# Kernel optimization log

Measured on AMD Instinct MI355X. Metric: run time of the kernel, lower is better.

## Reference

```python
import jax, jax.numpy as jnp
import numpy as np

N_NODES = 50000
N_EDGES = 1600000
N_GRAPHS = 512
VOCAB = 1000
EMB = 32
HID = 64
N_CLASS = 2


def setup_inputs() -> dict:
    key = jax.random.key(0)
    ks = jax.random.split(key, 12)
    x_ids = jax.random.randint(ks[0], (N_NODES,), 0, VOCAB)
    edge_index = jax.random.randint(ks[1], (2, N_EDGES), 0, N_NODES)
    batch = jnp.sort(jax.random.randint(ks[2], (N_NODES,), 0, N_GRAPHS))
    def s(k, shape, fan):
        return jax.random.normal(k, shape, jnp.float32) * (1.0 / np.sqrt(fan))
    return {
        "x_ids": x_ids,
        "edge_index": edge_index,
        "batch": batch,
        "embed": s(ks[3], (VOCAB, EMB), EMB),
        "w1_l": s(ks[4], (EMB, HID), EMB),
        "b1": jnp.zeros((HID,), jnp.float32),
        "w1_r": s(ks[5], (EMB, HID), EMB),
        "w2_l": s(ks[6], (HID, HID), HID),
        "b2": jnp.zeros((HID,), jnp.float32),
        "w2_r": s(ks[7], (HID, HID), HID),
        "w_out": s(ks[8], (HID, N_CLASS), HID),
        "b_out": jnp.zeros((N_CLASS,), jnp.float32),
    }


def _sage(x, src, dst, w_l, b, w_r):
    # PyG SAGEConv (aggr='mean'): out = lin_l(mean_{j in N(i)} x_j) + lin_r(x_i)
    msg_sum = jax.ops.segment_sum(x[src], dst, num_segments=N_NODES)  # [N, d]
    deg = jax.ops.segment_sum(jnp.ones((src.shape[0],), x.dtype), dst,
                              num_segments=N_NODES)
    mean = msg_sum / jnp.maximum(deg, 1.0)[:, None]
    return mean @ w_l + b + x @ w_r


def reference(x_ids, edge_index, batch, embed, w1_l, b1, w1_r,
              w2_l, b2, w2_r, w_out, b_out):
    src, dst = edge_index[0], edge_index[1]
    x = embed[x_ids]                                  # [N, emb]
    x = jax.nn.relu(_sage(x, src, dst, w1_l, b1, w1_r))  # [N, hid]
    x = jax.nn.relu(_sage(x, src, dst, w2_l, b2, w2_r))  # [N, hid]
    # global_mean_pool over batch segments
    gsum = jax.ops.segment_sum(x, batch, num_segments=N_GRAPHS)
    gcnt = jax.ops.segment_sum(jnp.ones((N_NODES,), x.dtype), batch,
                               num_segments=N_GRAPHS)
    pooled = gsum / jnp.maximum(gcnt, 1.0)[:, None]   # [G, hid]
    return pooled @ w_out + b_out                     # [G, n_class]
```

## Files before the change

### kernel.cpp

```cpp
#include <hip/hip_runtime.h>
#include <hip/hip_bf16.h>

#define N_NODES 50000
#define N_EDGES 1600000
#define N_GRAPHS 512
#define VOCAB 1000
#define EMB 32
#define HID 64
#define N_CLASS 2

#define MAXDEG 96

#define NVEC (N_EDGES / 4)
#define SORT_VPB 1024
#define SORT_BLOCKS ((NVEC + SORT_VPB - 1) / SORT_VPB)
#define BSHIFT 7
#define BUCKET_NODES 128
#define NBUCK ((N_NODES + BUCKET_NODES - 1) / BUCKET_NODES)

#define E1_BLOCKS ((VOCAB * HID + 255) / 256)

#define AGG_THREADS (N_NODES * 8)
#define AGG_BLOCKS ((AGG_THREADS + 255) / 256)

#define L2P_BLOCKS 768
#define L2P_WAVES (L2P_BLOCKS * 4)
#define L2P_CHUNK ((N_NODES + L2P_WAVES - 1) / L2P_WAVES)

typedef int iv4 __attribute__((ext_vector_type(4)));
typedef unsigned short us;
typedef us usv8 __attribute__((ext_vector_type(8)));
typedef float fv4 __attribute__((ext_vector_type(4)));
typedef unsigned long long u64;

__device__ __forceinline__ float bf2f(us u) {
    union { unsigned int i; float f; } c;
    c.i = ((unsigned int)u) << 16;
    return c.f;
}
__device__ __forceinline__ us f2bf(float f) {
    union { __hip_bfloat16 b; us u; } c;
    c.b = __float2bfloat16(f);
    return c.u;
}
__device__ __forceinline__ float rdlane(float v, int k) {
    return __int_as_float(__builtin_amdgcn_readlane(__float_as_int(v), k));
}

__global__ __launch_bounds__(256) void pre_hist_kernel(
        const int* __restrict__ dst, int* __restrict__ hist,
        const float* __restrict__ embed, const float* __restrict__ w1l,
        const float* __restrict__ w1r, us* __restrict__ e1b,
        float* __restrict__ e1r) {
    __shared__ int lh[NBUCK];
    if (blockIdx.x < SORT_BLOCKS) {
        for (int b = threadIdx.x; b < NBUCK; b += 256) lh[b] = 0;
        __syncthreads();
        const iv4* dst4 = (const iv4*)dst;
        int vbase = blockIdx.x * SORT_VPB;
        #pragma unroll
        for (int t = 0; t < 4; ++t) {
            int v = vbase + t * 256 + threadIdx.x;
            if (v < NVEC) {
                iv4 d4 = __builtin_nontemporal_load(&dst4[v]);
                atomicAdd(&lh[d4.x >> BSHIFT], 1);
                atomicAdd(&lh[d4.y >> BSHIFT], 1);
                atomicAdd(&lh[d4.z >> BSHIFT], 1);
                atomicAdd(&lh[d4.w >> BSHIFT], 1);
            }
        }
        __syncthreads();
        for (int b = threadIdx.x; b < NBUCK; b += 256)
            hist[b * SORT_BLOCKS + blockIdx.x] = lh[b];
    } else {
        int id = (blockIdx.x - SORT_BLOCKS) * 256 + threadIdx.x;
        if (id >= VOCAB * HID) return;
        int v = id >> 6, j = id & 63;
        float a = 0.0f, b = 0.0f;
        #pragma unroll
        for (int k = 0; k < EMB; ++k) {
            float ev = embed[v * EMB + k];
            a = fmaf(ev, w1l[k * HID + j], a);
            b = fmaf(ev, w1r[k * HID + j], b);
        }
        e1b[id] = f2bf(a);
        e1r[id] = b;
    }
}

__global__ __launch_bounds__(256) void scan_rows_kernel(int* __restrict__ hist,
                                                        int* __restrict__ btot) {
    int* row = hist + (size_t)blockIdx.x * SORT_BLOCKS;
    __shared__ int wsum[4];
    int tid = threadIdx.x, lane = tid & 63, w = tid >> 6;
    int carry = 0;
    for (int base = 0; base < SORT_BLOCKS; base += 256) {
        int idx = base + tid;
        int v = (idx < SORT_BLOCKS) ? row[idx] : 0;
        int inc = v;
        #pragma unroll
        for (int off = 1; off < 64; off <<= 1) {
            int n = __shfl_up(inc, off, 64);
            if (lane >= off) inc += n;
        }
        if (lane == 63) wsum[w] = inc;
        __syncthreads();
        int woff = 0;
        #pragma unroll
        for (int k = 0; k < 4; ++k) if (k < w) woff += wsum[k];
        if (idx < SORT_BLOCKS) row[idx] = carry + woff + inc - v;
        carry += wsum[0] + wsum[1] + wsum[2] + wsum[3];
        __syncthreads();
    }
    if (tid == 0) btot[blockIdx.x] = carry;
}

__global__ __launch_bounds__(256) void scatter_kernel(const int* __restrict__ src,
        const int* __restrict__ dst, const int* __restrict__ x_ids,
        const int* __restrict__ hist, const int* __restrict__ btot,
        int* __restrict__ boff, u64* __restrict__ ebuf) {
    __shared__ int lbase[NBUCK];
    __shared__ int wsum[4];
    int tid = threadIdx.x, lane = tid & 63, w = tid >> 6;
    int carry = 0;
    for (int base = 0; base < NBUCK; base += 256) {
        int idx = base + tid;
        int v = (idx < NBUCK) ? btot[idx] : 0;
        int inc = v;
        #pragma unroll
        for (int off = 1; off < 64; off <<= 1) {
            int n = __shfl_up(inc, off, 64);
            if (lane >= off) inc += n;
        }
        if (lane == 63) wsum[w] = inc;
        __syncthreads();
        int woff = 0;
        #pragma unroll
        for (int k = 0; k < 4; ++k) if (k < w) woff += wsum[k];
        if (idx < NBUCK) lbase[idx] = carry + woff + inc - v;
        carry += wsum[0] + wsum[1] + wsum[2] + wsum[3];
        __syncthreads();
    }
    for (int b = tid; b < NBUCK; b += 256) {
        if (blockIdx.x == 0) boff[b] = lbase[b];
        lbase[b] += hist[b * SORT_BLOCKS + blockIdx.x];
    }
    if (blockIdx.x == 0 && tid == 0) boff[NBUCK] = carry;
    __syncthreads();
    const iv4* dst4 = (const iv4*)dst;
    const iv4* src4 = (const iv4*)src;
    int vbase = blockIdx.x * SORT_VPB;
    #pragma unroll
    for (int t = 0; t < 4; ++t) {
        int v = vbase + t * 256 + threadIdx.x;
        if (v < NVEC) {
            iv4 d4 = __builtin_nontemporal_load(&dst4[v]);
            iv4 s4 = __builtin_nontemporal_load(&src4[v]);
            int pay0 = (x_ids[s4.x] << 16) | s4.x;
            int pay1 = (x_ids[s4.y] << 16) | s4.y;
            int pay2 = (x_ids[s4.z] << 16) | s4.z;
            int pay3 = (x_ids[s4.w] << 16) | s4.w;
            int p0 = atomicAdd(&lbase[d4.x >> BSHIFT], 1);
            int p1 = atomicAdd(&lbase[d4.y >> BSHIFT], 1);
            int p2 = atomicAdd(&lbase[d4.z >> BSHIFT], 1);
            int p3 = atomicAdd(&lbase[d4.w >> BSHIFT], 1);
            ebuf[p0] = ((u64)(unsigned)d4.x << 32) | (unsigned)pay0;
            ebuf[p1] = ((u64)(unsigned)d4.y << 32) | (unsigned)pay1;
            ebuf[p2] = ((u64)(unsigned)d4.z << 32) | (unsigned)pay2;
            ebuf[p3] = ((u64)(unsigned)d4.w << 32) | (unsigned)pay3;
        }
    }
}

__global__ __launch_bounds__(256) void csr_bucket_kernel(const u64* __restrict__ ebuf,
        const int* __restrict__ boff, int* __restrict__ cursor, int* __restrict__ csr,
        float* __restrict__ gsum) {
    int b = blockIdx.x;
    int tid = threadIdx.x;
    __shared__ int cur[BUCKET_NODES];
    for (int r = tid; r < BUCKET_NODES; r += 256) cur[r] = 0;
    if (b < 128) gsum[b * 256 + tid] = 0.0f;
    __syncthreads();
    int base = boff[b];
    int end  = boff[b + 1];
    int node0 = b << BSHIFT;
    for (int i = base + tid; i < end; i += 256) {
        u64 e = ebuf[i];
        int d = (int)(e >> 32);
        int pay = (int)(e & 0xffffffffu);
        int pos = atomicAdd(&cur[d - node0], 1);
        csr[(size_t)d * MAXDEG + pos] = pay;
    }
    __syncthreads();
    for (int r = tid; r < BUCKET_NODES; r += 256) {
        int d = node0 + r;
        if (d < N_NODES) cursor[d] = cur[r];
    }
}

__global__ __launch_bounds__(256) void agg1_lin1_kernel(
        const int* __restrict__ x_ids, const int* __restrict__ csr,
        const int* __restrict__ deg_arr, const us* __restrict__ e1b,
        const float* __restrict__ e1r, const float* __restrict__ b1,
        us* __restrict__ h1b) {
    int tid = blockIdx.x * blockDim.x + threadIdx.x;
    int lane = threadIdx.x & 63;
    int g = lane >> 3, c8 = lane & 7;
    int node = (tid >> 6) * 8 + g;
    bool valid = node < N_NODES;
    int nclamp = valid ? node : 0;
    int deg = valid ? deg_arr[nclamp] : 0;
    const int* crow = csr + (size_t)nclamp * MAXDEG;
    float a0=0.f,a1=0.f,a2=0.f,a3=0.f,a4=0.f,a5=0.f,a6=0.f,a7=0.f;
    for (int k = 0; k < deg; k += 4) {
        iv4 cv = *(const iv4*)(crow + k);
        #define GATH1(CVAL, T)                                                   \
        if (k + (T) < deg) {                                                     \
            int cls = (CVAL) >> 16;                                              \
            usv8 r = *(const usv8*)(e1b + cls * HID + c8 * 8);                   \
            a0 += bf2f(r[0]); a1 += bf2f(r[1]); a2 += bf2f(r[2]); a3 += bf2f(r[3]); \
            a4 += bf2f(r[4]); a5 += bf2f(r[5]); a6 += bf2f(r[6]); a7 += bf2f(r[7]); \
        }
        GATH1(cv.x, 0) GATH1(cv.y, 1) GATH1(cv.z, 2) GATH1(cv.w, 3)
        #undef GATH1
    }
    if (!valid) return;
    float inv = 1.0f / fmaxf((float)deg, 1.0f);
    int xid = x_ids[nclamp];
    const fv4* er = (const fv4*)(e1r + xid * HID + c8 * 8);
    fv4 e0 = er[0], e1v = er[1];
    const fv4* bb = (const fv4*)(b1 + c8 * 8);
    fv4 b0 = bb[0], b1v = bb[1];
    float h0 = fmaxf(a0 * inv + b0.x + e0.x, 0.0f);
    float h1 = fmaxf(a1 * inv + b0.y + e0.y, 0.0f);
    float h2 = fmaxf(a2 * inv + b0.z + e0.z, 0.0f);
    float h3 = fmaxf(a3 * inv + b0.w + e0.w, 0.0f);
    float h4 = fmaxf(a4 * inv + b1v.x + e1v.x, 0.0f);
    float h5 = fmaxf(a5 * inv + b1v.y + e1v.y, 0.0f);
    float h6 = fmaxf(a6 * inv + b1v.z + e1v.z, 0.0f);
    float h7 = fmaxf(a7 * inv + b1v.w + e1v.w, 0.0f);
    int o = node * HID + c8 * 8;
    usv8 hb;
    hb[0] = f2bf(h0); hb[1] = f2bf(h1); hb[2] = f2bf(h2); hb[3] = f2bf(h3);
    hb[4] = f2bf(h4); hb[5] = f2bf(h5); hb[6] = f2bf(h6); hb[7] = f2bf(h7);
    *(usv8*)(h1b + o) = hb;
}

__global__ __launch_bounds__(256) void agg2_mean_kernel(
        const us* __restrict__ h1b, const int* __restrict__ csr,
        const int* __restrict__ deg_arr, us* __restrict__ mean2b) {
    int tid = blockIdx.x * blockDim.x + threadIdx.x;
    int lane = threadIdx.x & 63;
    int g = lane >> 3, c8 = lane & 7;
    int node = (tid >> 6) * 8 + g;
    bool valid = node < N_NODES;
    int nclamp = valid ? node : 0;
    int deg = valid ? deg_arr[nclamp] : 0;
    const int* crow = csr + (size_t)nclamp * MAXDEG;
    float a0=0.f,a1=0.f,a2=0.f,a3=0.f,a4=0.f,a5=0.f,a6=0.f,a7=0.f;
    for (int k = 0; k < deg; k += 4) {
        iv4 cv = *(const iv4*)(crow + k);
        #define GATH2(CVAL, T)                                                   \
        if (k + (T) < deg) {                                                     \
            int nb = (CVAL) & 0xFFFF;                                            \
            usv8 r = *(const usv8*)(h1b + nb * HID + c8 * 8);                    \
            a0 += bf2f(r[0]); a1 += bf2f(r[1]); a2 += bf2f(r[2]); a3 += bf2f(r[3]); \
            a4 += bf2f(r[4]); a5 += bf2f(r[5]); a6 += bf2f(r[6]); a7 += bf2f(r[7]); \
        }
        GATH2(cv.x, 0) GATH2(cv.y, 1) GATH2(cv.z, 2) GATH2(cv.w, 3)
        #undef GATH2
    }
    if (!valid) return;
    float inv = 1.0f / fmaxf((float)deg, 1.0f);
    int o = node * HID + c8 * 8;
    usv8 mb;
    mb[0] = f2bf(a0 * inv); mb[1] = f2bf(a1 * inv);
    mb[2] = f2bf(a2 * inv); mb[3] = f2bf(a3 * inv);
    mb[4] = f2bf(a4 * inv); mb[5] = f2bf(a5 * inv);
    mb[6] = f2bf(a6 * inv); mb[7] = f2bf(a7 * inv);
    *(usv8*)(mean2b + o) = mb;
}

__global__ __launch_bounds__(256) void lin2_pool_kernel(
        const us* __restrict__ mean2b, const us* __restrict__ h1b,
        const float* __restrict__ w2l, const float* __restrict__ b2,
        const float* __restrict__ w2r, const int* __restrict__ batch,
        float* __restrict__ gsum) {
    int lane = threadIdx.x & 63;
    int wv = (blockIdx.x * blockDim.x + threadIdx.x) >> 6;
    int i0 = wv * L2P_CHUNK;
    int i1 = i0 + L2P_CHUNK; if (i1 > N_NODES) i1 = N_NODES;
    if (i0 >= N_NODES) return;
    float wl[HID], wr[HID];
    #pragma unroll
    for (int k = 0; k < HID; ++k) {
        wl[k] = w2l[k * HID + lane];
        wr[k] = w2r[k * HID + lane];
    }
    float bj = b2[lane];
    int curg = __builtin_amdgcn_readfirstlane(batch[i0]);
    float accp = 0.0f;
    float m = bf2f(mean2b[i0 * HID + lane]);
    float h = bf2f(h1b[i0 * HID + lane]);
    for (int i = i0; i < i1; ++i) {
        us mn_u = 0, hn_u = 0;
        if (i + 1 < i1) {
            mn_u = mean2b[(i + 1) * HID + lane];
            hn_u = h1b[(i + 1) * HID + lane];
        }
        int g = __builtin_amdgcn_readfirstlane(batch[i]);
        if (g != curg) {
            atomicAdd(&gsum[curg * HID + lane], accp);
            accp = 0.0f;
            curg = g;
        }
        float zm = 0.0f, zh = bj;
        #pragma unroll
        for (int k = 0; k < HID; ++k) {
            zm = fmaf(rdlane(m, k), wl[k], zm);
            zh = fmaf(rdlane(h, k), wr[k], zh);
        }
        accp += fmaxf(zm + zh, 0.0f);
        m = bf2f(mn_u); h = bf2f(hn_u);
    }
    atomicAdd(&gsum[curg * HID + lane], accp);
}

__global__ void out_kernel(const float* __restrict__ gsum, const int* __restrict__ batch,
                           const float* __restrict__ w_out, const float* __restrict__ b_out,
                           float* __restrict__ out) {
    int id = blockIdx.x * blockDim.x + threadIdx.x;
    if (id >= N_GRAPHS * N_CLASS) return;
    int g = id >> 1, c = id & 1;
    int lo = 0, hi = N_NODES;
    while (lo < hi) { int mid = (lo + hi) >> 1; if (batch[mid] < g) lo = mid + 1; else hi = mid; }
    int first = lo;
    lo = 0; hi = N_NODES;
    while (lo < hi) { int mid = (lo + hi) >> 1; if (batch[mid] <= g) lo = mid + 1; else hi = mid; }
    float cnt = (float)(lo - first);
    float inv = 1.0f / fmaxf(cnt, 1.0f);
    float acc = b_out[c];
    #pragma unroll
    for (int j = 0; j < HID; ++j)
        acc = fmaf(gsum[g * HID + j] * inv, w_out[j * N_CLASS + c], acc);
    out[id] = acc;
}


extern "C" void kernel_launch(void* const* d_in, const int* in_sizes, int n_in,
                              void* d_out, int out_size, void* d_ws, size_t ws_size,
                              hipStream_t stream) {
    const int*   x_ids = (const int*)d_in[0];
    const int*   edge  = (const int*)d_in[1];
    const int*   batch = (const int*)d_in[2];
    const float* embed = (const float*)d_in[3];
    const float* w1l   = (const float*)d_in[4];
    const float* b1    = (const float*)d_in[5];
    const float* w1r   = (const float*)d_in[6];
    const float* w2l   = (const float*)d_in[7];
    const float* b2    = (const float*)d_in[8];
    const float* w2r   = (const float*)d_in[9];
    const float* wout  = (const float*)d_in[10];
    const float* bout  = (const float*)d_in[11];
    const int* src = edge;
    const int* dst = edge + N_EDGES;
    float* out = (float*)d_out;

    char* ws = (char*)d_ws;
    size_t off = 0;
    auto alloc = [&](size_t bytes) -> void* {
        void* p = ws + off;
        off += (bytes + 255) & ~(size_t)255;
        return p;
    };
    us*     h1b    = (us*)alloc((size_t)N_NODES * HID * 2);
    u64*    ebuf   = (u64*)alloc((size_t)N_EDGES * 8);
    int*    csr    = (int*)alloc((size_t)N_NODES * MAXDEG * 4);
    int*    cursor = (int*)alloc((size_t)N_NODES * 4);
    int*    hist   = (int*)alloc((size_t)NBUCK * SORT_BLOCKS * 4);
    int*    btot   = (int*)alloc((size_t)NBUCK * 4);
    int*    boff   = (int*)alloc((size_t)(NBUCK + 1) * 4);
    us*     e1b    = (us*)alloc((size_t)VOCAB * HID * 2);
    float*  e1r    = (float*)alloc((size_t)VOCAB * HID * 4);
    float*  gsum   = (float*)alloc((size_t)N_GRAPHS * HID * 4);

    us* mean2b = (us*)ebuf;

    const int B = 256;
    pre_hist_kernel<<<SORT_BLOCKS + E1_BLOCKS, B, 0, stream>>>(dst, hist,
                                                               embed, w1l, w1r, e1b, e1r);
    scan_rows_kernel<<<NBUCK, B, 0, stream>>>(hist, btot);
    scatter_kernel<<<SORT_BLOCKS, B, 0, stream>>>(src, dst, x_ids, hist, btot, boff, ebuf);
    csr_bucket_kernel<<<NBUCK, B, 0, stream>>>(ebuf, boff, cursor, csr, gsum);
    agg1_lin1_kernel<<<AGG_BLOCKS, B, 0, stream>>>(x_ids, csr, cursor,
                                                   e1b, e1r, b1, h1b);
    agg2_mean_kernel<<<AGG_BLOCKS, B, 0, stream>>>(h1b, csr, cursor, mean2b);
    lin2_pool_kernel<<<L2P_BLOCKS, B, 0, stream>>>(mean2b, h1b, w2l, b2, w2r, batch, gsum);
    out_kernel<<<(N_GRAPHS * N_CLASS + B - 1) / B, B, 0, stream>>>(gsum, batch, wout, bout, out);
}
```

Measured before the change: 218.9 us.

## Stage scatter through shared-memory local sort for coalesced bucket writes

The scatter kernel now builds a per-block bucket histogram, does a local prefix scan, and sorts the block's edges into shared memory by bucket. It then writes them out contiguously using global bucket offsets, so consecutive threads write consecutive global addresses instead of issuing random 8-byte stores. The cost is an extra shared-memory histogram pass, another scan, and about 32KB of LDS per block, which may reduce occupancy.

```diff
diff --git a/kernel.cpp b/kernel.cpp
--- a/kernel.cpp
+++ b/kernel.cpp
@@ -13,6 +13,7 @@
 
 #define NVEC (N_EDGES / 4)
 #define SORT_VPB 1024
+#define SORT_EPB (SORT_VPB * 4)
 #define SORT_BLOCKS ((NVEC + SORT_VPB - 1) / SORT_VPB)
 #define BSHIFT 7
 #define BUCKET_NODES 128
@@ -119,10 +120,88 @@
         const int* __restrict__ dst, const int* __restrict__ x_ids,
         const int* __restrict__ hist, const int* __restrict__ btot,
         int* __restrict__ boff, u64* __restrict__ ebuf) {
-    __shared__ int lbase[NBUCK];
+    __shared__ u64 ebuf_l[SORT_EPB];
+    __shared__ int lh[NBUCK];
+    __shared__ int lstart[NBUCK];
+    __shared__ int lcur[NBUCK];
     __shared__ int wsum[4];
     int tid = threadIdx.x, lane = tid & 63, w = tid >> 6;
+    int blk = blockIdx.x;
+
+    const iv4* dst4 = (const iv4*)dst;
+    const iv4* src4 = (const iv4*)src;
+    int vbase = blk * SORT_VPB;
+    iv4 d4s[4], s4s[4];
+    bool vok[4];
+    #pragma unroll
+    for (int t = 0; t < 4; ++t) {
+        int v = vbase + t * 256 + tid;
+        vok[t] = (v < NVEC);
+        if (vok[t]) {
+            d4s[t] = __builtin_nontemporal_load(&dst4[v]);
+            s4s[t] = __builtin_nontemporal_load(&src4[v]);
+        }
+    }
+
+    for (int b = tid; b < NBUCK; b += 256) lh[b] = 0;
+    __syncthreads();
+    #pragma unroll
+    for (int t = 0; t < 4; ++t) {
+        if (vok[t]) {
+            atomicAdd(&lh[d4s[t].x >> BSHIFT], 1);
+            atomicAdd(&lh[d4s[t].y >> BSHIFT], 1);
+            atomicAdd(&lh[d4s[t].z >> BSHIFT], 1);
+            atomicAdd(&lh[d4s[t].w >> BSHIFT], 1);
+        }
+    }
+    __syncthreads();
+
     int carry = 0;
+    for (int base = 0; base < NBUCK; base += 256) {
+        int idx = base + tid;
+        int v = (idx < NBUCK) ? lh[idx] : 0;
+        int inc = v;
+        #pragma unroll
+        for (int off = 1; off < 64; off <<= 1) {
+            int n = __shfl_up(inc, off, 64);
+            if (lane >= off) inc += n;
+        }
+        if (lane == 63) wsum[w] = inc;
+        __syncthreads();
+        int woff = 0;
+        #pragma unroll
+        for (int k = 0; k < 4; ++k) if (k < w) woff += wsum[k];
+        if (idx < NBUCK) {
+            int ex = carry + woff + inc - v;
+            lstart[idx] = ex;
+            lcur[idx] = ex;
+        }
+        carry += wsum[0] + wsum[1] + wsum[2] + wsum[3];
+        __syncthreads();
+    }
+    int total = carry;
+
+    #pragma unroll
+    for (int t = 0; t < 4; ++t) {
+        if (vok[t]) {
+            iv4 d4 = d4s[t], s4 = s4s[t];
+            int pay0 = (x_ids[s4.x] << 16) | s4.x;
+            int pay1 = (x_ids[s4.y] << 16) | s4.y;
+            int pay2 = (x_ids[s4.z] << 16) | s4.z;
+            int pay3 = (x_ids[s4.w] << 16) | s4.w;
+            int p0 = atomicAdd(&lcur[d4.x >> BSHIFT], 1);
+            int p1 = atomicAdd(&lcur[d4.y >> BSHIFT], 1);
+            int p2 = atomicAdd(&lcur[d4.z >> BSHIFT], 1);
+            int p3 = atomicAdd(&lcur[d4.w >> BSHIFT], 1);
+            ebuf_l[p0] = ((u64)(unsigned)d4.x << 32) | (unsigned)pay0;
+            ebuf_l[p1] = ((u64)(unsigned)d4.y << 32) | (unsigned)pay1;
+            ebuf_l[p2] = ((u64)(unsigned)d4.z << 32) | (unsigned)pay2;
+            ebuf_l[p3] = ((u64)(unsigned)d4.w << 32) | (unsigned)pay3;
+        }
+    }
+    __syncthreads();
+
+    carry = 0;
     for (int base = 0; base < NBUCK; base += 256) {
         int idx = base + tid;
         int v = (idx < NBUCK) ? btot[idx] : 0;
@@ -137,38 +216,21 @@
         int woff = 0;
         #pragma unroll
         for (int k = 0; k < 4; ++k) if (k < w) woff += wsum[k];
-        if (idx < NBUCK) lbase[idx] = carry + woff + inc - v;
+        if (idx < NBUCK) {
+            int gb = carry + woff + inc - v;
+            if (blk == 0) boff[idx] = gb;
+            lh[idx] = gb + hist[idx * SORT_BLOCKS + blk] - lstart[idx];
+        }
         carry += wsum[0] + wsum[1] + wsum[2] + wsum[3];
         __syncthreads();
     }
-    for (int b = tid; b < NBUCK; b += 256) {
-        if (blockIdx.x == 0) boff[b] = lbase[b];
-        lbase[b] += hist[b * SORT_BLOCKS + blockIdx.x];
-    }
-    if (blockIdx.x == 0 && tid == 0) boff[NBUCK] = carry;
-    __syncthreads();
-    const iv4* dst4 = (const iv4*)dst;
-    const iv4* src4 = (const iv4*)src;
-    int vbase = blockIdx.x * SORT_VPB;
-    #pragma unroll
-    for (int t = 0; t < 4; ++t) {
-        int v = vbase + t * 256 + threadIdx.x;
-        if (v < NVEC) {
-            iv4 d4 = __builtin_nontemporal_load(&dst4[v]);
-            iv4 s4 = __builtin_nontemporal_load(&src4[v]);
-            int pay0 = (x_ids[s4.x] << 16) | s4.x;
-            int pay1 = (x_ids[s4.y] << 16) | s4.y;
-            int pay2 = (x_ids[s4.z] << 16) | s4.z;
-            int pay3 = (x_ids[s4.w] << 16) | s4.w;
-            int p0 = atomicAdd(&lbase[d4.x >> BSHIFT], 1);
-            int p1 = atomicAdd(&lbase[d4.y >> BSHIFT], 1);
-            int p2 = atomicAdd(&lbase[d4.z >> BSHIFT], 1);
-            int p3 = atomicAdd(&lbase[d4.w >> BSHIFT], 1);
-            ebuf[p0] = ((u64)(unsigned)d4.x << 32) | (unsigned)pay0;
-            ebuf[p1] = ((u64)(unsigned)d4.y << 32) | (unsigned)pay1;
-            ebuf[p2] = ((u64)(unsigned)d4.z << 32) | (unsigned)pay2;
-            ebuf[p3] = ((u64)(unsigned)d4.w << 32) | (unsigned)pay3;
-        }
+    if (blk == 0 && tid == 0) boff[NBUCK] = carry;
+    __syncthreads();
+
+    for (int i = tid; i < total; i += 256) {
+        u64 e = ebuf_l[i];
+        int b = (int)(e >> (32 + BSHIFT));
+        ebuf[lh[b] + i] = e;
     }
 }
 
```

Result: faster. 200.9 us (-8.2%).
